# Kernel tuning notes

Measured on AMD Instinct MI355X. Metric: run time of the kernel, lower is better.

The kernel has to match this reference:

```python
import jax, jax.numpy as jnp
import numpy as np

N = 100000      # nodes
E = 1600000     # edges (avg degree 16)
F_IN = 256      # Data.num_features
H = 128         # hidden_channels
C = 10          # num classes


def setup_inputs() -> dict:
    key = jax.random.key(0)
    ks = jax.random.split(key, 5)
    x = jax.random.normal(ks[0], (N, F_IN), dtype=jnp.float32)
    edge_index = jax.random.randint(ks[1], (2, E), 0, N, dtype=jnp.int32)
    W1 = jax.random.normal(ks[2], (F_IN, H), dtype=jnp.float32) / np.sqrt(F_IN)
    b1 = jnp.zeros((H,), dtype=jnp.float32)
    W2 = jax.random.normal(ks[3], (H, C), dtype=jnp.float32) / np.sqrt(H)
    b2 = jnp.zeros((C,), dtype=jnp.float32)
    return {"x": x, "edge_index": edge_index, "W1": W1, "b1": b1, "W2": W2, "b2": b2}


def _gcn_conv(x, W, b, src, dst, dinv_sqrt):
    # dense transform first (PyG GCNConv order), then normalized gather-scatter
    h = x @ W                                   # [N, out]
    norm = dinv_sqrt[src] * dinv_sqrt[dst]      # [E+N]
    msg = h[src] * norm[:, None]                # [E+N, out]
    out = jax.ops.segment_sum(msg, dst, num_segments=N)
    return out + b


def reference(x, edge_index, W1, b1, W2, b2):
    # add self-loops (GCNConv default)
    loop = jnp.arange(N, dtype=edge_index.dtype)
    src = jnp.concatenate([edge_index[0], loop])
    dst = jnp.concatenate([edge_index[1], loop])
    # symmetric normalization: D^-1/2 (A+I) D^-1/2, degree counted on dst
    deg = jax.ops.segment_sum(jnp.ones_like(dst, dtype=x.dtype), dst, num_segments=N)
    dinv_sqrt = jnp.where(deg > 0, jax.lax.rsqrt(deg), 0.0)
    h = _gcn_conv(x, W1, b1, src, dst, dinv_sqrt)
    h = jax.nn.relu(h)
    h = _gcn_conv(h, W2, b2, src, dst, dinv_sqrt)
    return jax.nn.log_softmax(h, axis=1)
```

## Files before the change

kernel.cpp:

```cpp
#include <hip/hip_runtime.h>
#include <math.h>

#define BLK 256
#define BKT_BITS 9
#define BKT (1<<BKT_BITS)
#define MAXNB 256
#define EB 8192

typedef __attribute__((ext_vector_type(8))) short bf16x8;
typedef __attribute__((ext_vector_type(4))) float f32x4;

__device__ inline unsigned short f2b(float f){
  union { float f; unsigned int u; } v; v.f = f;
  unsigned int u = v.u;
  return (unsigned short)((u + 0x7FFF + ((u >> 16) & 1)) >> 16);
}
__device__ inline float b2f_lo(unsigned int u){
  union { unsigned int u; float f; } v; v.u = u << 16; return v.f;
}
__device__ inline float b2f_hi(unsigned int u){
  union { unsigned int u; float f; } v; v.u = u & 0xFFFF0000u; return v.f;
}


__global__ __launch_bounds__(256)
void bhistA(const int* __restrict__ dst, int* __restrict__ bhist, int E, int NB){
  __shared__ int h[MAXNB];
  int t = threadIdx.x;
  for (int i=t;i<NB;i+=256) h[i]=0;
  __syncthreads();
  int base = blockIdx.x*EB;
  #pragma unroll
  for (int k=0;k<EB/256;k++){
    int idx = base + k*256 + t;
    if (idx < E) atomicAdd(&h[dst[idx]>>BKT_BITS], 1);
  }
  __syncthreads();
  for (int i=t;i<NB;i+=256) if (h[i]) atomicAdd(&bhist[i], h[i]);
}

__global__ __launch_bounds__(256)
void binC(const int* __restrict__ src, const int* __restrict__ dst,
          const int* __restrict__ bhist, int* __restrict__ bcur,
          unsigned int* __restrict__ bins, int E, int NB){
  __shared__ int hsc[MAXNB];
  __shared__ int lh[MAXNB];
  __shared__ int lofs[MAXNB];
  __shared__ int lcur[MAXNB];
  __shared__ int gres[MAXNB];
  __shared__ __attribute__((aligned(16))) int2 buf[EB];
  int t = threadIdx.x;
  int v0 = (t < NB) ? bhist[t] : 0;
  hsc[t] = v0;
  for (int i=t;i<NB;i+=256) lh[i]=0;
  __syncthreads();
  for (int off=1; off<MAXNB; off<<=1){
    int v = (t>=off)?hsc[t-off]:0;
    __syncthreads();
    hsc[t]+=v;
    __syncthreads();
  }
  int boff_t = hsc[t]-v0;
  int base = blockIdx.x*EB;
  #pragma unroll
  for (int k=0;k<EB/256;k++){
    int idx = base + k*256 + t;
    if (idx < E) atomicAdd(&lh[dst[idx]>>BKT_BITS], 1);
  }
  __syncthreads();
  if (t==0){ int run=0; for (int b=0;b<NB;b++){ lofs[b]=run; run+=lh[b]; } }
  __syncthreads();
  if (t<NB){
    lcur[t] = lofs[t];
    gres[t] = lh[t] ? (boff_t + atomicAdd(&bcur[t], lh[t])) : 0;
  }
  __syncthreads();
  #pragma unroll
  for (int k=0;k<EB/256;k++){
    int idx = base + k*256 + t;
    if (idx < E){
      int d = dst[idx];
      int p = atomicAdd(&lcur[d>>BKT_BITS], 1);
      buf[p] = make_int2(src[idx], d);
    }
  }
  __syncthreads();
  int total = E - base; if (total > EB) total = EB;
  for (int i=t; i<total; i+=256){
    int2 pr = buf[i];
    int b = pr.y>>BKT_BITS;
    bins[gres[b] + (i - lofs[b])] = ((unsigned)pr.x << BKT_BITS) | (unsigned)(pr.y & (BKT-1));
  }
}

__global__ __launch_bounds__(256)
void bfill_all(const unsigned int* __restrict__ bins, const int* __restrict__ bhist,
               int* __restrict__ rowptr, float* __restrict__ dinv, int* __restrict__ col,
               const float* __restrict__ W1, unsigned short* __restrict__ W1T,
               int N, int NB){
  int b = blockIdx.x;
  if (b >= NB){
    int t2 = (b - NB)*256 + threadIdx.x;
    if (t2 < 256*128){
      int k = t2 >> 7, n = t2 & 127;
      W1T[n*256 + k] = f2b(W1[t2]);
    }
    return;
  }
  __shared__ int dcnt[BKT];
  __shared__ int rp[BKT];
  __shared__ int cur[BKT];
  __shared__ int sscan[256];
  __shared__ int sboff;
  int t = threadIdx.x;
  int partial = 0;
  for (int j=t; j<b; j+=256) partial += bhist[j];
  if (t==0) sboff = 0;
  dcnt[t] = 0; dcnt[t+256] = 0;
  __syncthreads();
  if (partial) atomicAdd(&sboff, partial);
  __syncthreads();
  int s = sboff, cnt = bhist[b];
  for (int i=t;i<cnt;i+=256) atomicAdd(&dcnt[bins[s+i] & (BKT-1)], 1);
  __syncthreads();
  int base = b<<BKT_BITS;
  int i0 = 2*t, i1 = 2*t+1;
  int d0 = dcnt[i0], d1 = dcnt[i1];
  int n0 = (base+i0 < N) ? d0+1 : 0;
  int n1 = (base+i1 < N) ? d1+1 : 0;
  int tsum = n0+n1;
  sscan[t] = tsum; __syncthreads();
  for (int off=1; off<256; off<<=1){
    int v = (t>=off)? sscan[t-off]:0;
    __syncthreads();
    sscan[t]+=v;
    __syncthreads();
  }
  int run = sscan[t]-tsum;
  int gstart = s + base;
  int rp0 = gstart + run, rp1 = rp0 + n0;
  rp[i0] = rp0; rp[i1] = rp1;
  cur[i0] = 0;  cur[i1] = 0;
  if (base+i0 < N){
    rowptr[base+i0] = rp0;
    dinv[base+i0] = rsqrtf((float)(d0+1));
    if (base+i0 == N-1) rowptr[N] = rp0 + d0 + 1;
  }
  if (base+i1 < N){
    rowptr[base+i1] = rp1;
    dinv[base+i1] = rsqrtf((float)(d1+1));
    if (base+i1 == N-1) rowptr[N] = rp1 + d1 + 1;
  }
  __syncthreads();
  for (int i=t;i<cnt;i+=256){
    unsigned pk = bins[s+i];
    int ln = pk & (BKT-1);
    int slot = atomicAdd(&cur[ln], 1);
    col[rp[ln] + slot] = (int)(pk >> BKT_BITS);
  }
  __syncthreads();
  for (int i=t;i<BKT;i+=256){
    int node = base+i;
    if (node < N) col[rp[i] + dcnt[i]] = node;
  }
}


#define XPAD 40

__global__ __launch_bounds__(256)
void gemm1_mfma(const float* __restrict__ X, const unsigned short* __restrict__ W1T,
                const float* __restrict__ dinv, unsigned short* __restrict__ H1B, int M){
  __shared__ __attribute__((aligned(16))) unsigned short xs[128*XPAD];
  __shared__ __attribute__((aligned(16))) unsigned short wt[128*XPAD];
  const int tid = threadIdx.x;
  const int wave = tid >> 6, lane = tid & 63;
  const int quad = lane >> 4, l16 = lane & 15;
  const int row0 = blockIdx.x * 128;

  f32x4 acc[2][8];
  #pragma unroll
  for (int i=0;i<2;i++)
    #pragma unroll
    for (int j=0;j<8;j++) acc[i][j] = (f32x4){0.f,0.f,0.f,0.f};

  const int r    = tid >> 1;
  const int half = tid & 1;

  for (int k0 = 0; k0 < 256; k0 += 32){
    {
      int gr = row0 + r;
      const float* xp = X + (size_t)gr*256 + k0 + half*16;
      unsigned short* xd = xs + r*XPAD + half*16;
      #pragma unroll
      for (int q=0;q<4;q++){
        float4 v = (gr < M) ? *(const float4*)(xp + q*4) : make_float4(0.f,0.f,0.f,0.f);
        ushort4 b;
        b.x = f2b(v.x); b.y = f2b(v.y); b.z = f2b(v.z); b.w = f2b(v.w);
        *(ushort4*)(xd + q*4) = b;
      }
    }
    {
      const unsigned short* wp = W1T + r*256 + k0 + half*16;
      unsigned short* wd = wt + r*XPAD + half*16;
      uint4 a = *(const uint4*)wp;
      uint4 c = *(const uint4*)(wp + 8);
      *(uint4*)wd = a;
      *(uint4*)(wd + 8) = c;
    }
    __syncthreads();

    bf16x8 bfr[8];
    #pragma unroll
    for (int ct=0; ct<8; ct++)
      bfr[ct] = *(bf16x8*)(wt + (ct*16 + l16)*XPAD + quad*8);
    #pragma unroll
    for (int rt=0; rt<2; rt++){
      bf16x8 a = *(bf16x8*)(xs + (wave*32 + rt*16 + l16)*XPAD + quad*8);
      #pragma unroll
      for (int ct=0; ct<8; ct++)
        acc[rt][ct] = __builtin_amdgcn_mfma_f32_16x16x32_bf16(a, bfr[ct], acc[rt][ct], 0, 0, 0);
    }
    __syncthreads();
  }

  #pragma unroll
  for (int rt=0; rt<2; rt++){
    int rbase = row0 + wave*32 + rt*16 + quad*4;
    #pragma unroll
    for (int rg=0; rg<4; rg++){
      int grow = rbase + rg;
      if (grow < M){
        float dv = dinv[grow];
        #pragma unroll
        for (int ct=0; ct<8; ct++)
          H1B[(size_t)grow*128 + ct*16 + l16] = f2b(dv * acc[rt][ct][rg]);
      }
    }
  }
}


__device__ inline void acc8(float* a, uint4 u){
  a[0]+=b2f_lo(u.x); a[1]+=b2f_hi(u.x); a[2]+=b2f_lo(u.y); a[3]+=b2f_hi(u.y);
  a[4]+=b2f_lo(u.z); a[5]+=b2f_hi(u.z); a[6]+=b2f_lo(u.w); a[7]+=b2f_hi(u.w);
}

__global__ __launch_bounds__(256)
void agg1_kernel(const unsigned short* __restrict__ H1B, const int* __restrict__ rowptr,
                 const int* __restrict__ col, const float* __restrict__ dinv,
                 const float* __restrict__ b1, unsigned int* __restrict__ R1B, int N){
  int node = blockIdx.x * 4 + (threadIdx.x >> 6);
  int lane = threadIdx.x & 63;
  int g   = lane >> 4;
  int l16 = lane & 15;
  if (node >= N) return;
  int s = rowptr[node], e = rowptr[node+1];
  float a[8];
  #pragma unroll
  for (int k=0;k<8;k++) a[k]=0.f;
  const char* hbase = (const char*)H1B + l16*16;
  int j = s;
  for (; j+15 < e; j+=16){
    int c0 = col[j+g], c1 = col[j+4+g], c2 = col[j+8+g], c3 = col[j+12+g];
    uint4 u0 = *(const uint4*)(hbase + (((unsigned)c0) << 8));
    uint4 u1 = *(const uint4*)(hbase + (((unsigned)c1) << 8));
    uint4 u2 = *(const uint4*)(hbase + (((unsigned)c2) << 8));
    uint4 u3 = *(const uint4*)(hbase + (((unsigned)c3) << 8));
    acc8(a, u0); acc8(a, u1); acc8(a, u2); acc8(a, u3);
  }
  for (; j+7 < e; j+=8){
    int c0 = col[j+g], c1 = col[j+4+g];
    uint4 u0 = *(const uint4*)(hbase + (((unsigned)c0) << 8));
    uint4 u1 = *(const uint4*)(hbase + (((unsigned)c1) << 8));
    acc8(a, u0); acc8(a, u1);
  }
  {
    int rem = e - j;
    if (g < rem){
      int c0 = col[j+g];
      uint4 u0 = *(const uint4*)(hbase + (((unsigned)c0) << 8));
      acc8(a, u0);
    }
    if (g+4 < rem){
      int c1 = col[j+4+g];
      uint4 u1 = *(const uint4*)(hbase + (((unsigned)c1) << 8));
      acc8(a, u1);
    }
  }
  #pragma unroll
  for (int k=0;k<8;k++){
    a[k] += __shfl_xor(a[k], 16);
    a[k] += __shfl_xor(a[k], 32);
  }
  if (g == 0){
    float dv = dinv[node];
    float4 bl = *(const float4*)(b1 + l16*8);
    float4 bh = *(const float4*)(b1 + l16*8 + 4);
    float f0, f1;
    unsigned int o0, o1, o2, o3;
    f0 = fmaxf(dv*a[0] + bl.x, 0.f); f1 = fmaxf(dv*a[1] + bl.y, 0.f);
    o0 = (unsigned)f2b(f0) | ((unsigned)f2b(f1) << 16);
    f0 = fmaxf(dv*a[2] + bl.z, 0.f); f1 = fmaxf(dv*a[3] + bl.w, 0.f);
    o1 = (unsigned)f2b(f0) | ((unsigned)f2b(f1) << 16);
    f0 = fmaxf(dv*a[4] + bh.x, 0.f); f1 = fmaxf(dv*a[5] + bh.y, 0.f);
    o2 = (unsigned)f2b(f0) | ((unsigned)f2b(f1) << 16);
    f0 = fmaxf(dv*a[6] + bh.z, 0.f); f1 = fmaxf(dv*a[7] + bh.w, 0.f);
    o3 = (unsigned)f2b(f0) | ((unsigned)f2b(f1) << 16);
    *(uint4*)(R1B + (size_t)node*64 + l16*4) = make_uint4(o0, o1, o2, o3);
  }
}


__global__ __launch_bounds__(256)
void gemm2_kernel(const unsigned int* __restrict__ R1B, const float* __restrict__ W2,
                  const float* __restrict__ dinv, unsigned int* __restrict__ H2B, int M){
  __shared__ float w2s[128*10];
  for (int i = threadIdx.x; i < 128*10; i += blockDim.x) w2s[i] = W2[i];
  __syncthreads();
  int r = blockIdx.x*blockDim.x + threadIdx.x;
  if (r >= M) return;
  float acc[10];
  #pragma unroll
  for (int c=0;c<10;c++) acc[c] = 0.f;
  const unsigned int* row = R1B + (size_t)r*64;
  for (int k=0;k<64;k+=4){
    uint4 u = *(const uint4*)(row + k);
    float f0 = b2f_lo(u.x), f1 = b2f_hi(u.x);
    float f2 = b2f_lo(u.y), f3 = b2f_hi(u.y);
    float f4 = b2f_lo(u.z), f5 = b2f_hi(u.z);
    float f6 = b2f_lo(u.w), f7 = b2f_hi(u.w);
    #pragma unroll
    for (int c=0;c<10;c++){
      acc[c] += f0*w2s[(2*k+0)*10+c] + f1*w2s[(2*k+1)*10+c]
              + f2*w2s[(2*k+2)*10+c] + f3*w2s[(2*k+3)*10+c]
              + f4*w2s[(2*k+4)*10+c] + f5*w2s[(2*k+5)*10+c]
              + f6*w2s[(2*k+6)*10+c] + f7*w2s[(2*k+7)*10+c];
    }
  }
  float dv = dinv[r];
  unsigned int p[5];
  #pragma unroll
  for (int c=0;c<5;c++)
    p[c] = (unsigned)f2b(dv*acc[2*c]) | ((unsigned)f2b(dv*acc[2*c+1]) << 16);
  unsigned int* op = H2B + (size_t)r*8;
  *(uint4*)op = make_uint4(p[0],p[1],p[2],p[3]);
  op[4] = p[4];
}


__global__ __launch_bounds__(256)
void agg2_softmax_kernel(const unsigned int* __restrict__ H2B, const int* __restrict__ rowptr,
                         const int* __restrict__ col, const float* __restrict__ dinv,
                         const float* __restrict__ b2, float* __restrict__ out, int N){
  int i = blockIdx.x*blockDim.x + threadIdx.x;
  if (i >= N) return;
  float acc[10], acc2[10];
  #pragma unroll
  for (int c=0;c<10;c++){ acc[c] = 0.f; acc2[c] = 0.f; }
  int s = rowptr[i], e = rowptr[i+1];
  int j = s;
  for (; j+1 < e; j += 2){
    const unsigned int* hA = H2B + (size_t)col[j]*8;
    const unsigned int* hB = H2B + (size_t)col[j+1]*8;
    uint4 a = *(const uint4*)hA; unsigned a4 = hA[4];
    uint4 b = *(const uint4*)hB; unsigned b4 = hB[4];
    acc[0]+=b2f_lo(a.x); acc[1]+=b2f_hi(a.x); acc[2]+=b2f_lo(a.y); acc[3]+=b2f_hi(a.y);
    acc[4]+=b2f_lo(a.z); acc[5]+=b2f_hi(a.z); acc[6]+=b2f_lo(a.w); acc[7]+=b2f_hi(a.w);
    acc[8]+=b2f_lo(a4);  acc[9]+=b2f_hi(a4);
    acc2[0]+=b2f_lo(b.x); acc2[1]+=b2f_hi(b.x); acc2[2]+=b2f_lo(b.y); acc2[3]+=b2f_hi(b.y);
    acc2[4]+=b2f_lo(b.z); acc2[5]+=b2f_hi(b.z); acc2[6]+=b2f_lo(b.w); acc2[7]+=b2f_hi(b.w);
    acc2[8]+=b2f_lo(b4);  acc2[9]+=b2f_hi(b4);
  }
  if (j < e){
    const unsigned int* hA = H2B + (size_t)col[j]*8;
    uint4 a = *(const uint4*)hA; unsigned a4 = hA[4];
    acc[0]+=b2f_lo(a.x); acc[1]+=b2f_hi(a.x); acc[2]+=b2f_lo(a.y); acc[3]+=b2f_hi(a.y);
    acc[4]+=b2f_lo(a.z); acc[5]+=b2f_hi(a.z); acc[6]+=b2f_lo(a.w); acc[7]+=b2f_hi(a.w);
    acc[8]+=b2f_lo(a4);  acc[9]+=b2f_hi(a4);
  }
  float dv = dinv[i];
  #pragma unroll
  for (int f=0;f<10;f++) acc[f] = dv*(acc[f] + acc2[f]) + b2[f];
  float m = acc[0];
  #pragma unroll
  for (int f=1;f<10;f++) m = fmaxf(m, acc[f]);
  float sum = 0.f;
  #pragma unroll
  for (int f=0;f<10;f++) sum += expf(acc[f] - m);
  float lg = m + logf(sum);
  #pragma unroll
  for (int f=0;f<10;f++) out[(size_t)i*10 + f] = acc[f] - lg;
}


extern "C" void kernel_launch(void* const* d_in, const int* in_sizes, int n_in,
                              void* d_out, int out_size, void* d_ws, size_t ws_size,
                              hipStream_t stream){
  const float* x    = (const float*)d_in[0];
  const int*   ei   = (const int*)d_in[1];
  const float* W1   = (const float*)d_in[2];
  const float* b1   = (const float*)d_in[3];
  const float* W2   = (const float*)d_in[4];
  const float* b2   = (const float*)d_in[5];
  float* out = (float*)d_out;

  const int N = in_sizes[0] / 256;
  const int E = in_sizes[1] / 2;
  const int NNZ = E + N;
  const int* src = ei;
  const int* dst = ei + E;
  const int NB = (N + BKT - 1) >> BKT_BITS;
  const int WB = 128;

  char* ws = (char*)d_ws;
  size_t off = 0;
  auto alloc = [&](size_t bytes)->char*{
    char* p = ws + off;
    off = (off + bytes + 255) & ~(size_t)255;
    return p;
  };
  int*   zreg   = (int*)  alloc((size_t)(MAXNB*2)*4);
  int*   bhist  = zreg;
  int*   bcur   = zreg + MAXNB;
  float* dinv   = (float*)alloc((size_t)N*4);
  int*   rowptr = (int*)  alloc((size_t)(N+1)*4);
  unsigned int* bins = (unsigned int*)alloc((size_t)E*4);
  int*   col    = (int*)  alloc((size_t)NNZ*4);
  unsigned short* w1t = (unsigned short*)alloc((size_t)128*256*2);
  unsigned short* h1b = (unsigned short*)alloc((size_t)N*128*2);
  unsigned int*   r1b = (unsigned int*)  alloc((size_t)N*64*4);
  unsigned int*   h2b = (unsigned int*)  alloc((size_t)N*8*4);
  (void)ws_size;

  hipMemsetAsync(zreg, 0, (size_t)(MAXNB*2)*4, stream);

  const int NCB = (E + EB - 1) / EB;

  bhistA<<<NCB, 256, 0, stream>>>(dst, bhist, E, NB);
  binC<<<NCB, 256, 0, stream>>>(src, dst, bhist, bcur, bins, E, NB);
  bfill_all<<<NB + WB, 256, 0, stream>>>(bins, bhist, rowptr, dinv, col, W1, w1t, N, NB);

  gemm1_mfma<<<(N+127)/128, 256, 0, stream>>>(x, w1t, dinv, h1b, N);
  agg1_kernel<<<(N+3)/4, 256, 0, stream>>>(h1b, rowptr, col, dinv, b1, r1b, N);
  gemm2_kernel<<<(N+BLK-1)/BLK, BLK, 0, stream>>>(r1b, W2, dinv, h2b, N);
  agg2_softmax_kernel<<<(N+BLK-1)/BLK, BLK, 0, stream>>>(h2b, rowptr, col, dinv, b2, out, N);
}
```

Baseline: 360.5 us.

## Double-buffer LDS tiles and register-prefetch next K slice in gemm1

The first GEMM now keeps two LDS buffers for the X and W tiles and loads the next K-slice from global memory into registers while the current slice is computed with MFMA. The trailing barrier per iteration is removed because the alternating buffers separate writes from reads. The goal is to hide global load latency behind compute and halve the barriers. In exchange it doubles LDS use, which may lower occupancy, and raises register pressure from the prefetched values.

```diff
diff --git a/kernel.cpp b/kernel.cpp
--- a/kernel.cpp
+++ b/kernel.cpp
@@ -171,8 +171,8 @@
 __global__ __launch_bounds__(256)
 void gemm1_mfma(const float* __restrict__ X, const unsigned short* __restrict__ W1T,
                 const float* __restrict__ dinv, unsigned short* __restrict__ H1B, int M){
-  __shared__ __attribute__((aligned(16))) unsigned short xs[128*XPAD];
-  __shared__ __attribute__((aligned(16))) unsigned short wt[128*XPAD];
+  __shared__ __attribute__((aligned(16))) unsigned short xs[2][128*XPAD];
+  __shared__ __attribute__((aligned(16))) unsigned short wt[2][128*XPAD];
   const int tid = threadIdx.x;
   const int wave = tid >> 6, lane = tid & 63;
   const int quad = lane >> 4, l16 = lane & 15;
@@ -186,42 +186,57 @@
 
   const int r    = tid >> 1;
   const int half = tid & 1;
-
-  for (int k0 = 0; k0 < 256; k0 += 32){
+  const int gr = row0 + r;
+  const bool rok = gr < M;
+  const float* xp = X + (size_t)gr*256 + half*16;
+  const unsigned short* wp = W1T + r*256 + half*16;
+
+  float4 xv[4];
+  uint4  wv[2];
+  #pragma unroll
+  for (int q=0;q<4;q++)
+    xv[q] = rok ? *(const float4*)(xp + q*4) : make_float4(0.f,0.f,0.f,0.f);
+  wv[0] = *(const uint4*)wp;
+  wv[1] = *(const uint4*)(wp + 8);
+
+  #pragma unroll
+  for (int t=0; t<8; t++){
+    const int k0 = t*32;
+    const int pb = t & 1;
     {
-      int gr = row0 + r;
-      const float* xp = X + (size_t)gr*256 + k0 + half*16;
-      unsigned short* xd = xs + r*XPAD + half*16;
+      unsigned short* xd = xs[pb] + r*XPAD + half*16;
       #pragma unroll
       for (int q=0;q<4;q++){
-        float4 v = (gr < M) ? *(const float4*)(xp + q*4) : make_float4(0.f,0.f,0.f,0.f);
         ushort4 b;
-        b.x = f2b(v.x); b.y = f2b(v.y); b.z = f2b(v.z); b.w = f2b(v.w);
+        b.x = f2b(xv[q].x); b.y = f2b(xv[q].y); b.z = f2b(xv[q].z); b.w = f2b(xv[q].w);
         *(ushort4*)(xd + q*4) = b;
       }
-    }
-    {
-      const unsigned short* wp = W1T + r*256 + k0 + half*16;
-      unsigned short* wd = wt + r*XPAD + half*16;
-      uint4 a = *(const uint4*)wp;
-      uint4 c = *(const uint4*)(wp + 8);
-      *(uint4*)wd = a;
-      *(uint4*)(wd + 8) = c;
+      unsigned short* wd = wt[pb] + r*XPAD + half*16;
+      *(uint4*)wd = wv[0];
+      *(uint4*)(wd + 8) = wv[1];
+    }
+    if (t < 7){
+      const float* xp2 = xp + k0 + 32;
+      #pragma unroll
+      for (int q=0;q<4;q++)
+        xv[q] = rok ? *(const float4*)(xp2 + q*4) : make_float4(0.f,0.f,0.f,0.f);
+      const unsigned short* wp2 = wp + k0 + 32;
+      wv[0] = *(const uint4*)wp2;
+      wv[1] = *(const uint4*)(wp2 + 8);
     }
     __syncthreads();
 
     bf16x8 bfr[8];
     #pragma unroll
     for (int ct=0; ct<8; ct++)
-      bfr[ct] = *(bf16x8*)(wt + (ct*16 + l16)*XPAD + quad*8);
+      bfr[ct] = *(bf16x8*)(wt[pb] + (ct*16 + l16)*XPAD + quad*8);
     #pragma unroll
     for (int rt=0; rt<2; rt++){
-      bf16x8 a = *(bf16x8*)(xs + (wave*32 + rt*16 + l16)*XPAD + quad*8);
+      bf16x8 a = *(bf16x8*)(xs[pb] + (wave*32 + rt*16 + l16)*XPAD + quad*8);
       #pragma unroll
       for (int ct=0; ct<8; ct++)
         acc[rt][ct] = __builtin_amdgcn_mfma_f32_16x16x32_bf16(a, bfr[ct], acc[rt][ct], 0, 0, 0);
     }
-    __syncthreads();
   }
 
   #pragma unroll
```

Result: no change. 365.2 us (+1.3%).

## Load X straight into MFMA fragments with register double-buffering and preload full W1

Applied to the files above, without the earlier changes.

The first GEMM no longer stages X tiles through shared memory with per-K-step barriers. Each lane now loads its X fragment directly from global memory into registers, using a two-stage prefetch, and converts it with packed bf16 conversion instructions. The whole W1 matrix is preloaded once into shared memory in fragment order, so the K loop has no barriers. In exchange it uses 64KB of LDS per block, which may limit occupancy, and global X reads become less coalesced.

```diff
diff --git a/kernel.cpp b/kernel.cpp
--- a/kernel.cpp
+++ b/kernel.cpp
@@ -20,6 +20,11 @@
 }
 __device__ inline float b2f_hi(unsigned int u){
   union { unsigned int u; float f; } v; v.u = u & 0xFFFF0000u; return v.f;
+}
+__device__ inline unsigned pkbf(float lo, float hi){
+  unsigned r;
+  asm("v_cvt_pk_bf16_f32 %0, %1, %2" : "=v"(r) : "v"(lo), "v"(hi));
+  return r;
 }
 
 
@@ -166,17 +171,30 @@
 }
 
 
-#define XPAD 40
-
 __global__ __launch_bounds__(256)
 void gemm1_mfma(const float* __restrict__ X, const unsigned short* __restrict__ W1T,
                 const float* __restrict__ dinv, unsigned short* __restrict__ H1B, int M){
-  __shared__ __attribute__((aligned(16))) unsigned short xs[128*XPAD];
-  __shared__ __attribute__((aligned(16))) unsigned short wt[128*XPAD];
+  __shared__ __attribute__((aligned(16))) unsigned short wsh[64*512];
   const int tid = threadIdx.x;
   const int wave = tid >> 6, lane = tid & 63;
   const int quad = lane >> 4, l16 = lane & 15;
-  const int row0 = blockIdx.x * 128;
+
+  #pragma unroll
+  for (int f0=0; f0<64; f0+=4){
+    int f = f0 + wave;
+    int ct = f >> 3, ts = f & 7;
+    uint4 v = *(const uint4*)(W1T + (ct*16 + l16)*256 + ts*32 + quad*8);
+    *(uint4*)(wsh + f*512 + lane*8) = v;
+  }
+  __syncthreads();
+
+  const int row0 = blockIdx.x * 128 + wave * 32;
+  int rA = row0 + l16;
+  int rB = rA + 16;
+  int rAc = (rA < M) ? rA : (M-1);
+  int rBc = (rB < M) ? rB : (M-1);
+  const float* xA = X + (size_t)rAc*256 + quad*8;
+  const float* xB = X + (size_t)rBc*256 + quad*8;
 
   f32x4 acc[2][8];
   #pragma unroll
@@ -184,49 +202,44 @@
     #pragma unroll
     for (int j=0;j<8;j++) acc[i][j] = (f32x4){0.f,0.f,0.f,0.f};
 
-  const int r    = tid >> 1;
-  const int half = tid & 1;
-
-  for (int k0 = 0; k0 < 256; k0 += 32){
-    {
-      int gr = row0 + r;
-      const float* xp = X + (size_t)gr*256 + k0 + half*16;
-      unsigned short* xd = xs + r*XPAD + half*16;
-      #pragma unroll
-      for (int q=0;q<4;q++){
-        float4 v = (gr < M) ? *(const float4*)(xp + q*4) : make_float4(0.f,0.f,0.f,0.f);
-        ushort4 b;
-        b.x = f2b(v.x); b.y = f2b(v.y); b.z = f2b(v.z); b.w = f2b(v.w);
-        *(ushort4*)(xd + q*4) = b;
-      }
-    }
-    {
-      const unsigned short* wp = W1T + r*256 + k0 + half*16;
-      unsigned short* wd = wt + r*XPAD + half*16;
-      uint4 a = *(const uint4*)wp;
-      uint4 c = *(const uint4*)(wp + 8);
-      *(uint4*)wd = a;
-      *(uint4*)(wd + 8) = c;
-    }
-    __syncthreads();
-
-    bf16x8 bfr[8];
+  float4 pf[2][4];
+  #pragma unroll
+  for (int s=0;s<2;s++){
+    pf[s][0] = *(const float4*)(xA + s*32);
+    pf[s][1] = *(const float4*)(xA + s*32 + 4);
+    pf[s][2] = *(const float4*)(xB + s*32);
+    pf[s][3] = *(const float4*)(xB + s*32 + 4);
+  }
+
+  #pragma unroll
+  for (int t=0; t<8; t++){
+    const int cur = t & 1;
+    union { bf16x8 v; unsigned u[4]; } fa, fb;
+    fa.u[0] = pkbf(pf[cur][0].x, pf[cur][0].y);
+    fa.u[1] = pkbf(pf[cur][0].z, pf[cur][0].w);
+    fa.u[2] = pkbf(pf[cur][1].x, pf[cur][1].y);
+    fa.u[3] = pkbf(pf[cur][1].z, pf[cur][1].w);
+    fb.u[0] = pkbf(pf[cur][2].x, pf[cur][2].y);
+    fb.u[1] = pkbf(pf[cur][2].z, pf[cur][2].w);
+    fb.u[2] = pkbf(pf[cur][3].x, pf[cur][3].y);
+    fb.u[3] = pkbf(pf[cur][3].z, pf[cur][3].w);
+    if (t < 6){
+      pf[cur][0] = *(const float4*)(xA + (t+2)*32);
+      pf[cur][1] = *(const float4*)(xA + (t+2)*32 + 4);
+      pf[cur][2] = *(const float4*)(xB + (t+2)*32);
+      pf[cur][3] = *(const float4*)(xB + (t+2)*32 + 4);
+    }
     #pragma unroll
-    for (int ct=0; ct<8; ct++)
-      bfr[ct] = *(bf16x8*)(wt + (ct*16 + l16)*XPAD + quad*8);
-    #pragma unroll
-    for (int rt=0; rt<2; rt++){
-      bf16x8 a = *(bf16x8*)(xs + (wave*32 + rt*16 + l16)*XPAD + quad*8);
-      #pragma unroll
-      for (int ct=0; ct<8; ct++)
-        acc[rt][ct] = __builtin_amdgcn_mfma_f32_16x16x32_bf16(a, bfr[ct], acc[rt][ct], 0, 0, 0);
-    }
-    __syncthreads();
+    for (int ct=0; ct<8; ct++){
+      bf16x8 bf = *(const bf16x8*)(wsh + (ct*8 + t)*512 + lane*8);
+      acc[0][ct] = __builtin_amdgcn_mfma_f32_16x16x32_bf16(fa.v, bf, acc[0][ct], 0, 0, 0);
+      acc[1][ct] = __builtin_amdgcn_mfma_f32_16x16x32_bf16(fb.v, bf, acc[1][ct], 0, 0, 0);
+    }
   }
 
   #pragma unroll
   for (int rt=0; rt<2; rt++){
-    int rbase = row0 + wave*32 + rt*16 + quad*4;
+    int rbase = row0 + rt*16 + quad*4;
     #pragma unroll
     for (int rg=0; rg<4; rg++){
       int grow = rbase + rg;
```

Result: no change. 358.9 us (-0.5%).
